# Kernel optimization log

Hardware: AMD Instinct MI355X
Metric: run time of the kernel (lower is better)

Reference implementation:

```python
import jax, jax.numpy as jnp
import numpy as np

N_NODES = 50000
N_EDGES = 500000
FEAT = 64
HEADS = 4


def setup_inputs() -> dict:
    key = jax.random.key(0)
    ks = jax.random.split(key, 8)
    x = jax.random.normal(ks[0], (N_NODES, FEAT), jnp.float32)
    edge_index = jax.random.randint(ks[1], (2, N_EDGES), 0, N_NODES)
    edge_vec = jax.random.normal(ks[2], (N_EDGES, 3), jnp.float32)
    edge_len = jax.random.uniform(ks[3], (N_EDGES,), jnp.float32)
    # learned parameters
    w_proj = jax.random.normal(ks[4], (HEADS, FEAT, FEAT), jnp.float32) / np.float32(np.sqrt(FEAT))
    xav = np.float32(np.sqrt(6.0 / (HEADS + FEAT)))
    radial_score = jax.random.uniform(ks[5], (HEADS, FEAT), jnp.float32, -xav, xav)
    tangential_score = jax.random.uniform(ks[6], (HEADS, FEAT), jnp.float32, -xav, xav)
    radial_distance_scale = jnp.array(1.0, jnp.float32)
    w_out = jax.random.normal(ks[7], (FEAT, FEAT), jnp.float32) / np.float32(np.sqrt(FEAT))
    return {
        "x": x,
        "edge_index": edge_index,
        "edge_vec": edge_vec,
        "edge_len": edge_len,
        "w_proj": w_proj,
        "radial_score": radial_score,
        "tangential_score": tangential_score,
        "radial_distance_scale": radial_distance_scale,
        "w_out": w_out,
    }


def reference(x, edge_index, edge_vec, edge_len, w_proj, radial_score,
              tangential_score, radial_distance_scale, w_out):
    # edge_vec is accepted by the original forward but never used.
    sender, receiver = edge_index[0], edge_index[1]
    num_nodes = x.shape[0]
    # per-head projection: [N,H,F]
    proj = jnp.einsum('nf,hfg->nhg', x, w_proj)
    # edge deltas: [E,H,F]
    delta = proj[sender] - proj[receiver]
    # logits: [E,H]
    radial_logits = jnp.einsum('ehf,hf->eh', delta, radial_score) \
        - radial_distance_scale * edge_len[:, None]
    tangential_logits = jnp.einsum('ehf,hf->eh', delta, tangential_score)

    def seg_softmax_msg(logits):
        # segment softmax over edges grouped by receiver (equivalent to the
        m = jax.ops.segment_max(logits, receiver, num_segments=num_nodes)  # [N,H]
        e = jnp.exp(logits - m[receiver])                                  # [E,H]
        s = jax.ops.segment_sum(e, receiver, num_segments=num_nodes)      # [N,H]
        alpha = e / s[receiver]                                            # [E,H]
        # weighted scatter-sum of deltas -> [N,H,F]
        return jax.ops.segment_sum(alpha[:, :, None] * delta, receiver,
                                   num_segments=num_nodes)

    out = (seg_softmax_msg(radial_logits) + seg_softmax_msg(tangential_logits))
    out = out.mean(axis=1)  # mean over heads -> [N,F]
    out = jnp.nan_to_num(out)
    return x + out @ w_out
```

## Files before the change

### kernel.cpp

```cpp
#include <hip/hip_runtime.h>

#define NN 50000
#define NE 500000
#define CAP 40

static __device__ __forceinline__ unsigned short f2b(float f) {
    union { float f; unsigned int u; } v; v.f = f;
    unsigned int u = v.u;
    unsigned int r = (u + 0x7FFFu + ((u >> 16) & 1u)) >> 16;
    return (unsigned short)r;
}
static __device__ __forceinline__ float b2f(unsigned short b) {
    union { unsigned int u; float f; } v; v.u = ((unsigned int)b) << 16;
    return v.f;
}
static __device__ __forceinline__ unsigned int pack2(float a, float b) {
    return (unsigned int)f2b(a) | ((unsigned int)f2b(b) << 16);
}

static __device__ __forceinline__ void finish_node(
    int n, float4 a, float4 r4, float4 t4, int lane, int h, int gq,
    float2* __restrict__ rst, unsigned short* __restrict__ projb)
{
    float pr = a.x * r4.x + a.y * r4.y + a.z * r4.z + a.w * r4.w;
    float pt = a.x * t4.x + a.y * t4.y + a.z * t4.z + a.w * t4.w;
    #pragma unroll
    for (int m = 1; m < 16; m <<= 1) {
        pr += __shfl_xor(pr, m);
        pt += __shfl_xor(pt, m);
    }
    if (gq == 0) rst[n * 4 + h] = make_float2(pr, pt);
    ushort4 pb;
    pb.x = f2b(a.x); pb.y = f2b(a.y); pb.z = f2b(a.z); pb.w = f2b(a.w);
    *((ushort4*)(projb + (size_t)n * 256 + lane * 4)) = pb;
}

__global__ __launch_bounds__(256) void k_proj(
    const float* __restrict__ x, const float* __restrict__ wp,
    const float* __restrict__ rsc, const float* __restrict__ tsc,
    unsigned short* __restrict__ projb, float2* __restrict__ rst,
    int* __restrict__ cnt)
{
    __shared__ float lw[4 * 64 * 64];
    int tid = threadIdx.x;
    int gtid = blockIdx.x * 256 + tid;
    if (gtid < NN) cnt[gtid] = 0;
    for (int i = tid; i < 4096; i += 256)
        ((float4*)lw)[i] = ((const float4*)wp)[i];
    __syncthreads();

    int lane = tid & 63, wid = tid >> 6;
    int h = lane >> 4, gq = lane & 15;
    const float4* wrow = (const float4*)(lw + h * 4096);
    float4 r4 = *(const float4*)(rsc + h * 64 + gq * 4);
    float4 t4 = *(const float4*)(tsc + h * 64 + gq * 4);

    int gw = blockIdx.x * 4 + wid;
    int n0 = gw * 4;
    if (n0 >= NN) return;
    float xv0 = x[(n0 + 0) * 64 + lane];
    float xv1 = x[(n0 + 1) * 64 + lane];
    float xv2 = x[(n0 + 2) * 64 + lane];
    float xv3 = x[(n0 + 3) * 64 + lane];
    float4 a0 = {0,0,0,0}, a1 = {0,0,0,0}, a2 = {0,0,0,0}, a3 = {0,0,0,0};
    #pragma unroll 4
    for (int k = 0; k < 64; ++k) {
        float4 w4 = wrow[k * 16 + gq];
        float k0 = __shfl(xv0, k), k1 = __shfl(xv1, k);
        float k2 = __shfl(xv2, k), k3 = __shfl(xv3, k);
        a0.x += k0 * w4.x; a0.y += k0 * w4.y; a0.z += k0 * w4.z; a0.w += k0 * w4.w;
        a1.x += k1 * w4.x; a1.y += k1 * w4.y; a1.z += k1 * w4.z; a1.w += k1 * w4.w;
        a2.x += k2 * w4.x; a2.y += k2 * w4.y; a2.z += k2 * w4.z; a2.w += k2 * w4.w;
        a3.x += k3 * w4.x; a3.y += k3 * w4.y; a3.z += k3 * w4.z; a3.w += k3 * w4.w;
    }
    finish_node(n0 + 0, a0, r4, t4, lane, h, gq, rst, projb);
    finish_node(n0 + 1, a1, r4, t4, lane, h, gq, rst, projb);
    finish_node(n0 + 2, a2, r4, t4, lane, h, gq, rst, projb);
    finish_node(n0 + 3, a3, r4, t4, lane, h, gq, rst, projb);
}

__global__ __launch_bounds__(256) void k_bucket(
    const int* __restrict__ ei, const float* __restrict__ elen,
    const float* __restrict__ rst_f,
    const float* __restrict__ scale_p,
    int* __restrict__ cnt, int* __restrict__ ssend, uint4* __restrict__ scrh)
{
    int e = blockIdx.x * 256 + threadIdx.x;
    if (e >= NE) return;
    int s = ei[e], r = ei[NE + e];
    float d = scale_p[0] * elen[e];
    float4 ss0 = *(const float4*)(rst_f + s * 8);
    float4 ss1 = *(const float4*)(rst_f + s * 8 + 4);
    float4 rr0 = *(const float4*)(rst_f + r * 8);
    float4 rr1 = *(const float4*)(rst_f + r * 8 + 4);
    int slot = atomicAdd(&cnt[r], 1);
    if (slot >= CAP) return;
    int idx = r * CAP + slot;
    ssend[idx] = s;
    uint4 rec;
    rec.x = pack2(__expf(ss0.x - rr0.x - d), __expf(ss0.y - rr0.y));
    rec.y = pack2(__expf(ss0.z - rr0.z - d), __expf(ss0.w - rr0.w));
    rec.z = pack2(__expf(ss1.x - rr1.x - d), __expf(ss1.y - rr1.y));
    rec.w = pack2(__expf(ss1.z - rr1.z - d), __expf(ss1.w - rr1.w));
    scrh[idx] = rec;
}

__global__ __launch_bounds__(256, 8) void k_msg(
    const float* __restrict__ x, const unsigned short* __restrict__ projb,
    const int* __restrict__ cnt, const int* __restrict__ ssend,
    const unsigned int* __restrict__ scrh_u,
    const float* __restrict__ wout, float* __restrict__ out)
{
    __shared__ float lwT[64 * 68];
    int tid = threadIdx.x;
    for (int i = tid; i < 4096; i += 256) {
        int f = i >> 6, g = i & 63;
        lwT[g * 68 + f] = wout[i];
    }

    int lane = tid & 63, wid = tid >> 6;
    int h = lane >> 4, q = lane & 15, grp = h << 4;
    int n = blockIdx.x * 4 + wid;

    float outv = x[n * 64 + lane];
    int cn = cnt[n]; if (cn > CAP) cn = CAP;

    float4 ar = {0.f,0.f,0.f,0.f}, at = {0.f,0.f,0.f,0.f};
    float srl = 0.f, stl = 0.f;

#define ROWLD(SJ) (*(const ushort4*)(projb + ((size_t)(SJ) << 8) + (lane << 2)))
#define CONS(P, IDX) { \
    float cr = __shfl(erq, grp + (IDX)); \
    float ct = __shfl(etq, grp + (IDX)); \
    float p0 = b2f((P).x), p1 = b2f((P).y), p2 = b2f((P).z), p3 = b2f((P).w); \
    ar.x += cr * p0; ar.y += cr * p1; ar.z += cr * p2; ar.w += cr * p3; \
    at.x += ct * p0; at.y += ct * p1; at.z += ct * p2; at.w += ct * p3; }

    if (cn > 0) {
        int rowb = n * CAP;
        for (int base = 0; base < cn; base += 12) {
            int bc = cn - base; if (bc > 12) bc = 12;
            int sv = ssend[rowb + base + q];
            unsigned cw = scrh_u[(size_t)(rowb + base + q) * 4 + h];
            int sq = (q < bc) ? sv : n;
            float erq = 0.f, etq = 0.f;
            if (q < bc) {
                erq = b2f((unsigned short)(cw & 0xffff));
                etq = b2f((unsigned short)(cw >> 16));
            }
            srl += erq; stl += etq;
            ushort4 pA = ROWLD(__shfl(sq, 0));
            ushort4 pB = ROWLD(__shfl(sq, 1));
            ushort4 pC = ROWLD(__shfl(sq, 2));
            ushort4 pD = ROWLD(__shfl(sq, 3));
            ushort4 pE = ROWLD(__shfl(sq, 4));
            ushort4 pF = ROWLD(__shfl(sq, 5));
            ushort4 pG = ROWLD(__shfl(sq, 6));
            ushort4 pH = ROWLD(__shfl(sq, 7));
            ushort4 pI = ROWLD(__shfl(sq, 8));
            ushort4 pJ = ROWLD(__shfl(sq, 9));
            ushort4 pK = ROWLD(__shfl(sq, 10));
            ushort4 pL = ROWLD(__shfl(sq, 11));
            CONS(pA, 0)  CONS(pB, 1)  CONS(pC, 2)  CONS(pD, 3)
            CONS(pE, 4)  CONS(pF, 5)  CONS(pG, 6)  CONS(pH, 7)
            CONS(pI, 8)  CONS(pJ, 9)  CONS(pK, 10) CONS(pL, 11)
        }
        #pragma unroll
        for (int m = 1; m < 16; m <<= 1) {
            srl += __shfl_xor(srl, m);
            stl += __shfl_xor(stl, m);
        }
        float isr = 1.0f / srl, ist = 1.0f / stl;
        ushort4 pr = ROWLD(n);
        ar.x = isr * ar.x + ist * at.x - 2.f * b2f(pr.x);
        ar.y = isr * ar.y + ist * at.y - 2.f * b2f(pr.y);
        ar.z = isr * ar.z + ist * at.z - 2.f * b2f(pr.z);
        ar.w = isr * ar.w + ist * at.w - 2.f * b2f(pr.w);
    }
    ar.x += __shfl_xor(ar.x, 16); ar.y += __shfl_xor(ar.y, 16);
    ar.z += __shfl_xor(ar.z, 16); ar.w += __shfl_xor(ar.w, 16);
    ar.x += __shfl_xor(ar.x, 32); ar.y += __shfl_xor(ar.y, 32);
    ar.z += __shfl_xor(ar.z, 32); ar.w += __shfl_xor(ar.w, 32);
    float4 m4 = make_float4(0.25f * ar.x, 0.25f * ar.y, 0.25f * ar.z, 0.25f * ar.w);

    __syncthreads();

    const float* wTg = lwT + lane * 68;
    #pragma unroll
    for (int j = 0; j < 16; ++j) {
        float4 wv = *(const float4*)(wTg + j * 4);
        outv += __shfl(m4.x, j) * wv.x + __shfl(m4.y, j) * wv.y
              + __shfl(m4.z, j) * wv.z + __shfl(m4.w, j) * wv.w;
    }
    out[n * 64 + lane] = outv;
#undef ROWLD
#undef CONS
}

extern "C" void kernel_launch(void* const* d_in, const int* in_sizes, int n_in,
                              void* d_out, int out_size, void* d_ws, size_t ws_size,
                              hipStream_t stream) {
    const float* x       = (const float*)d_in[0];
    const int*   ei      = (const int*)d_in[1];
    const float* elen    = (const float*)d_in[3];
    const float* wp      = (const float*)d_in[4];
    const float* rsc     = (const float*)d_in[5];
    const float* tsc     = (const float*)d_in[6];
    const float* scale_p = (const float*)d_in[7];
    const float* wout    = (const float*)d_in[8];
    float* out = (float*)d_out;

    char* ws = (char*)d_ws;
    size_t off = 0;
    auto alloc = [&](size_t bytes) {
        void* p = ws + off;
        off = (off + bytes + 255) & ~(size_t)255;
        return p;
    };
    unsigned short* projb = (unsigned short*)alloc((size_t)NN * 256 * 2);
    float2* rst   = (float2*)alloc((size_t)NN * 4 * 8);
    int*    cnt   = (int*)alloc((size_t)NN * 4);
    int*    ssend = (int*)alloc(((size_t)NN * CAP + 64) * 4);
    uint4*  scrh  = (uint4*)alloc(((size_t)NN * CAP + 64) * 16);

    k_proj<<<3125, 256, 0, stream>>>(x, wp, rsc, tsc, projb, rst, cnt);
    k_bucket<<<(NE + 255) / 256, 256, 0, stream>>>(ei, elen, (const float*)rst,
                                                   scale_p, cnt, ssend, scrh);
    k_msg<<<12500, 256, 0, stream>>>(x, projb, cnt, ssend,
                                     (const unsigned int*)scrh, wout, out);
}
```

Measured before the change: 271.7 us.

## Fuse projection, bucketing and message passing into one persistent grid-barrier kernel

```diff
diff --git a/kernel.cpp b/kernel.cpp
--- a/kernel.cpp
+++ b/kernel.cpp
@@ -3,12 +3,15 @@
 #define NN 50000
 #define NE 500000
 #define CAP 40
+#define NBLK 1024
+#define NTHR 256
+#define GSTRIDE (NBLK * NTHR)
+#define NWAVES (NBLK * 4)
 
 static __device__ __forceinline__ unsigned short f2b(float f) {
     union { float f; unsigned int u; } v; v.f = f;
     unsigned int u = v.u;
-    unsigned int r = (u + 0x7FFFu + ((u >> 16) & 1u)) >> 16;
-    return (unsigned short)r;
+    return (unsigned short)((u + 0x7FFFu + ((u >> 16) & 1u)) >> 16);
 }
 static __device__ __forceinline__ float b2f(unsigned short b) {
     union { unsigned int u; float f; } v; v.u = ((unsigned int)b) << 16;
@@ -18,115 +21,107 @@
     return (unsigned int)f2b(a) | ((unsigned int)f2b(b) << 16);
 }
 
-static __device__ __forceinline__ void finish_node(
-    int n, float4 a, float4 r4, float4 t4, int lane, int h, int gq,
-    float2* __restrict__ rst, unsigned short* __restrict__ projb)
-{
-    float pr = a.x * r4.x + a.y * r4.y + a.z * r4.z + a.w * r4.w;
-    float pt = a.x * t4.x + a.y * t4.y + a.z * t4.z + a.w * t4.w;
-    #pragma unroll
-    for (int m = 1; m < 16; m <<= 1) {
-        pr += __shfl_xor(pr, m);
-        pt += __shfl_xor(pt, m);
-    }
-    if (gq == 0) rst[n * 4 + h] = make_float2(pr, pt);
-    ushort4 pb;
-    pb.x = f2b(a.x); pb.y = f2b(a.y); pb.z = f2b(a.z); pb.w = f2b(a.w);
-    *((ushort4*)(projb + (size_t)n * 256 + lane * 4)) = pb;
-}
-
-__global__ __launch_bounds__(256) void k_proj(
-    const float* __restrict__ x, const float* __restrict__ wp,
+static __device__ __forceinline__ void grid_barrier(int* bar, int target) {
+    __syncthreads();
+    if (threadIdx.x == 0) {
+        __threadfence();
+        __hip_atomic_fetch_add(bar, 1, __ATOMIC_RELEASE, __HIP_MEMORY_SCOPE_AGENT);
+        while (__hip_atomic_load(bar, __ATOMIC_RELAXED, __HIP_MEMORY_SCOPE_AGENT) < target)
+            __builtin_amdgcn_s_sleep(8);
+        (void)__hip_atomic_load(bar, __ATOMIC_ACQUIRE, __HIP_MEMORY_SCOPE_AGENT);
+        __threadfence();
+    }
+    __syncthreads();
+}
+
+__global__ __launch_bounds__(NTHR, 4) void k_fused(
+    const float* __restrict__ x, const int* __restrict__ ei,
+    const float* __restrict__ elen, const float* __restrict__ wp,
     const float* __restrict__ rsc, const float* __restrict__ tsc,
+    const float* __restrict__ scale_p, const float* __restrict__ wout,
     unsigned short* __restrict__ projb, float2* __restrict__ rst,
-    int* __restrict__ cnt)
-{
-    __shared__ float lw[4 * 64 * 64];
-    int tid = threadIdx.x;
-    int gtid = blockIdx.x * 256 + tid;
-    if (gtid < NN) cnt[gtid] = 0;
-    for (int i = tid; i < 4096; i += 256)
-        ((float4*)lw)[i] = ((const float4*)wp)[i];
-    __syncthreads();
-
-    int lane = tid & 63, wid = tid >> 6;
-    int h = lane >> 4, gq = lane & 15;
-    const float4* wrow = (const float4*)(lw + h * 4096);
-    float4 r4 = *(const float4*)(rsc + h * 64 + gq * 4);
-    float4 t4 = *(const float4*)(tsc + h * 64 + gq * 4);
-
-    int gw = blockIdx.x * 4 + wid;
-    int n0 = gw * 4;
-    if (n0 >= NN) return;
-    float xv0 = x[(n0 + 0) * 64 + lane];
-    float xv1 = x[(n0 + 1) * 64 + lane];
-    float xv2 = x[(n0 + 2) * 64 + lane];
-    float xv3 = x[(n0 + 3) * 64 + lane];
-    float4 a0 = {0,0,0,0}, a1 = {0,0,0,0}, a2 = {0,0,0,0}, a3 = {0,0,0,0};
-    #pragma unroll 4
-    for (int k = 0; k < 64; ++k) {
-        float4 w4 = wrow[k * 16 + gq];
-        float k0 = __shfl(xv0, k), k1 = __shfl(xv1, k);
-        float k2 = __shfl(xv2, k), k3 = __shfl(xv3, k);
-        a0.x += k0 * w4.x; a0.y += k0 * w4.y; a0.z += k0 * w4.z; a0.w += k0 * w4.w;
-        a1.x += k1 * w4.x; a1.y += k1 * w4.y; a1.z += k1 * w4.z; a1.w += k1 * w4.w;
-        a2.x += k2 * w4.x; a2.y += k2 * w4.y; a2.z += k2 * w4.z; a2.w += k2 * w4.w;
-        a3.x += k3 * w4.x; a3.y += k3 * w4.y; a3.z += k3 * w4.z; a3.w += k3 * w4.w;
-    }
-    finish_node(n0 + 0, a0, r4, t4, lane, h, gq, rst, projb);
-    finish_node(n0 + 1, a1, r4, t4, lane, h, gq, rst, projb);
-    finish_node(n0 + 2, a2, r4, t4, lane, h, gq, rst, projb);
-    finish_node(n0 + 3, a3, r4, t4, lane, h, gq, rst, projb);
-}
-
-__global__ __launch_bounds__(256) void k_bucket(
-    const int* __restrict__ ei, const float* __restrict__ elen,
-    const float* __restrict__ rst_f,
-    const float* __restrict__ scale_p,
-    int* __restrict__ cnt, int* __restrict__ ssend, uint4* __restrict__ scrh)
-{
-    int e = blockIdx.x * 256 + threadIdx.x;
-    if (e >= NE) return;
-    int s = ei[e], r = ei[NE + e];
-    float d = scale_p[0] * elen[e];
-    float4 ss0 = *(const float4*)(rst_f + s * 8);
-    float4 ss1 = *(const float4*)(rst_f + s * 8 + 4);
-    float4 rr0 = *(const float4*)(rst_f + r * 8);
-    float4 rr1 = *(const float4*)(rst_f + r * 8 + 4);
-    int slot = atomicAdd(&cnt[r], 1);
-    if (slot >= CAP) return;
-    int idx = r * CAP + slot;
-    ssend[idx] = s;
-    uint4 rec;
-    rec.x = pack2(__expf(ss0.x - rr0.x - d), __expf(ss0.y - rr0.y));
-    rec.y = pack2(__expf(ss0.z - rr0.z - d), __expf(ss0.w - rr0.w));
-    rec.z = pack2(__expf(ss1.x - rr1.x - d), __expf(ss1.y - rr1.y));
-    rec.w = pack2(__expf(ss1.z - rr1.z - d), __expf(ss1.w - rr1.w));
-    scrh[idx] = rec;
-}
-
-__global__ __launch_bounds__(256, 8) void k_msg(
-    const float* __restrict__ x, const unsigned short* __restrict__ projb,
-    const int* __restrict__ cnt, const int* __restrict__ ssend,
-    const unsigned int* __restrict__ scrh_u,
-    const float* __restrict__ wout, float* __restrict__ out)
+    int* __restrict__ cnt, int* __restrict__ ssend,
+    unsigned int* __restrict__ scrh_u, int* __restrict__ bar,
+    float* __restrict__ out)
 {
     __shared__ float lwT[64 * 68];
-    int tid = threadIdx.x;
-    for (int i = tid; i < 4096; i += 256) {
+    const int tid = threadIdx.x, bid = blockIdx.x;
+    const int gtid = bid * NTHR + tid;
+    const int lane = tid & 63, wid = tid >> 6;
+    const int wgid = bid * 4 + wid;
+    const int h = lane >> 4, q = lane & 15, grp = h << 4;
+
+    for (int i = gtid; i < NN; i += GSTRIDE) cnt[i] = 0;
+    {
+        const float4* wrow = (const float4*)(wp + (size_t)h * 4096);
+        float4 r4 = *(const float4*)(rsc + h * 64 + q * 4);
+        float4 t4 = *(const float4*)(tsc + h * 64 + q * 4);
+        for (int g8 = wgid; g8 < NN / 8; g8 += NWAVES) {
+            int n0 = g8 * 8;
+            float xv[8]; float4 a[8];
+            #pragma unroll
+            for (int j = 0; j < 8; ++j) {
+                xv[j] = x[(n0 + j) * 64 + lane];
+                a[j] = make_float4(0.f, 0.f, 0.f, 0.f);
+            }
+            #pragma unroll 4
+            for (int k = 0; k < 64; ++k) {
+                float4 w4 = wrow[k * 16 + q];
+                #pragma unroll
+                for (int j = 0; j < 8; ++j) {
+                    float kx = __shfl(xv[j], k);
+                    a[j].x += kx * w4.x; a[j].y += kx * w4.y;
+                    a[j].z += kx * w4.z; a[j].w += kx * w4.w;
+                }
+            }
+            #pragma unroll
+            for (int j = 0; j < 8; ++j) {
+                int n = n0 + j;
+                float pr = a[j].x * r4.x + a[j].y * r4.y + a[j].z * r4.z + a[j].w * r4.w;
+                float pt = a[j].x * t4.x + a[j].y * t4.y + a[j].z * t4.z + a[j].w * t4.w;
+                #pragma unroll
+                for (int m = 1; m < 16; m <<= 1) {
+                    pr += __shfl_xor(pr, m);
+                    pt += __shfl_xor(pt, m);
+                }
+                if (q == 0) rst[n * 4 + h] = make_float2(pr, pt);
+                ushort4 pb;
+                pb.x = f2b(a[j].x); pb.y = f2b(a[j].y);
+                pb.z = f2b(a[j].z); pb.w = f2b(a[j].w);
+                *((ushort4*)(projb + (size_t)n * 256 + lane * 4)) = pb;
+            }
+        }
+    }
+    grid_barrier(bar, NBLK);
+
+    {
+        float sc = scale_p[0];
+        const float* sf = (const float*)rst;
+        for (int e = gtid; e < NE; e += GSTRIDE) {
+            int s = ei[e], r = ei[NE + e];
+            float d = sc * elen[e];
+            float4 ss0 = *(const float4*)(sf + s * 8);
+            float4 ss1 = *(const float4*)(sf + s * 8 + 4);
+            int slot = atomicAdd(&cnt[r], 1);
+            if (slot < CAP) {
+                int idx = r * CAP + slot;
+                ssend[idx] = s;
+                uint4 rec;
+                rec.x = pack2(__expf(ss0.x - d), __expf(ss0.y));
+                rec.y = pack2(__expf(ss0.z - d), __expf(ss0.w));
+                rec.z = pack2(__expf(ss1.x - d), __expf(ss1.y));
+                rec.w = pack2(__expf(ss1.z - d), __expf(ss1.w));
+                *((uint4*)(scrh_u + (size_t)idx * 4)) = rec;
+            }
+        }
+    }
+    grid_barrier(bar, 2 * NBLK);
+
+    for (int i = tid; i < 4096; i += NTHR) {
         int f = i >> 6, g = i & 63;
         lwT[g * 68 + f] = wout[i];
     }
-
-    int lane = tid & 63, wid = tid >> 6;
-    int h = lane >> 4, q = lane & 15, grp = h << 4;
-    int n = blockIdx.x * 4 + wid;
-
-    float outv = x[n * 64 + lane];
-    int cn = cnt[n]; if (cn > CAP) cn = CAP;
-
-    float4 ar = {0.f,0.f,0.f,0.f}, at = {0.f,0.f,0.f,0.f};
-    float srl = 0.f, stl = 0.f;
+    __syncthreads();
 
 #define ROWLD(SJ) (*(const ushort4*)(projb + ((size_t)(SJ) << 8) + (lane << 2)))
 #define CONS(P, IDX) { \
@@ -136,63 +131,70 @@
     ar.x += cr * p0; ar.y += cr * p1; ar.z += cr * p2; ar.w += cr * p3; \
     at.x += ct * p0; at.y += ct * p1; at.z += ct * p2; at.w += ct * p3; }
 
-    if (cn > 0) {
-        int rowb = n * CAP;
-        for (int base = 0; base < cn; base += 12) {
-            int bc = cn - base; if (bc > 12) bc = 12;
-            int sv = ssend[rowb + base + q];
-            unsigned cw = scrh_u[(size_t)(rowb + base + q) * 4 + h];
-            int sq = (q < bc) ? sv : n;
-            float erq = 0.f, etq = 0.f;
-            if (q < bc) {
-                erq = b2f((unsigned short)(cw & 0xffff));
-                etq = b2f((unsigned short)(cw >> 16));
-            }
-            srl += erq; stl += etq;
-            ushort4 pA = ROWLD(__shfl(sq, 0));
-            ushort4 pB = ROWLD(__shfl(sq, 1));
-            ushort4 pC = ROWLD(__shfl(sq, 2));
-            ushort4 pD = ROWLD(__shfl(sq, 3));
-            ushort4 pE = ROWLD(__shfl(sq, 4));
-            ushort4 pF = ROWLD(__shfl(sq, 5));
-            ushort4 pG = ROWLD(__shfl(sq, 6));
-            ushort4 pH = ROWLD(__shfl(sq, 7));
-            ushort4 pI = ROWLD(__shfl(sq, 8));
-            ushort4 pJ = ROWLD(__shfl(sq, 9));
-            ushort4 pK = ROWLD(__shfl(sq, 10));
-            ushort4 pL = ROWLD(__shfl(sq, 11));
-            CONS(pA, 0)  CONS(pB, 1)  CONS(pC, 2)  CONS(pD, 3)
-            CONS(pE, 4)  CONS(pF, 5)  CONS(pG, 6)  CONS(pH, 7)
-            CONS(pI, 8)  CONS(pJ, 9)  CONS(pK, 10) CONS(pL, 11)
-        }
+    for (int n = wgid; n < NN; n += NWAVES) {
+        float outv = x[n * 64 + lane];
+        int cn = __hip_atomic_load(&cnt[n], __ATOMIC_RELAXED, __HIP_MEMORY_SCOPE_AGENT);
+        if (cn > CAP) cn = CAP;
+        float4 ar = {0.f,0.f,0.f,0.f}, at = {0.f,0.f,0.f,0.f};
+        float srl = 0.f, stl = 0.f;
+        if (cn > 0) {
+            int rowb = n * CAP;
+            for (int base = 0; base < cn; base += 12) {
+                int bc = cn - base; if (bc > 12) bc = 12;
+                int idx = rowb + base + ((q < bc) ? q : (bc - 1));
+                int sq = __hip_atomic_load(&ssend[idx], __ATOMIC_RELAXED,
+                                           __HIP_MEMORY_SCOPE_AGENT);
+                unsigned cw = __hip_atomic_load(&scrh_u[(size_t)idx * 4 + h],
+                                                __ATOMIC_RELAXED, __HIP_MEMORY_SCOPE_AGENT);
+                float erq = 0.f, etq = 0.f;
+                if (q < bc) {
+                    erq = b2f((unsigned short)(cw & 0xffff));
+                    etq = b2f((unsigned short)(cw >> 16));
+                }
+                srl += erq; stl += etq;
+                ushort4 pA = ROWLD(__shfl(sq, 0));
+                ushort4 pB = ROWLD(__shfl(sq, 1));
+                ushort4 pC = ROWLD(__shfl(sq, 2));
+                ushort4 pD = ROWLD(__shfl(sq, 3));
+                ushort4 pE = ROWLD(__shfl(sq, 4));
+                ushort4 pF = ROWLD(__shfl(sq, 5));
+                ushort4 pG = ROWLD(__shfl(sq, 6));
+                ushort4 pH = ROWLD(__shfl(sq, 7));
+                ushort4 pI = ROWLD(__shfl(sq, 8));
+                ushort4 pJ = ROWLD(__shfl(sq, 9));
+                ushort4 pK = ROWLD(__shfl(sq, 10));
+                ushort4 pL = ROWLD(__shfl(sq, 11));
+                CONS(pA, 0)  CONS(pB, 1)  CONS(pC, 2)  CONS(pD, 3)
+                CONS(pE, 4)  CONS(pF, 5)  CONS(pG, 6)  CONS(pH, 7)
+                CONS(pI, 8)  CONS(pJ, 9)  CONS(pK, 10) CONS(pL, 11)
+            }
+            #pragma unroll
+            for (int m = 1; m < 16; m <<= 1) {
+                srl += __shfl_xor(srl, m);
+                stl += __shfl_xor(stl, m);
+            }
+            float isr = 1.0f / srl, ist = 1.0f / stl;
+            ushort4 pr = ROWLD(n);
+            ar.x = isr * ar.x + ist * at.x - 2.f * b2f(pr.x);
+            ar.y = isr * ar.y + ist * at.y - 2.f * b2f(pr.y);
+            ar.z = isr * ar.z + ist * at.z - 2.f * b2f(pr.z);
+            ar.w = isr * ar.w + ist * at.w - 2.f * b2f(pr.w);
+        }
+        ar.x += __shfl_xor(ar.x, 16); ar.y += __shfl_xor(ar.y, 16);
+        ar.z += __shfl_xor(ar.z, 16); ar.w += __shfl_xor(ar.w, 16);
+        ar.x += __shfl_xor(ar.x, 32); ar.y += __shfl_xor(ar.y, 32);
+        ar.z += __shfl_xor(ar.z, 32); ar.w += __shfl_xor(ar.w, 32);
+        float4 m4 = make_float4(0.25f * ar.x, 0.25f * ar.y, 0.25f * ar.z, 0.25f * ar.w);
+
+        const float* wTg = lwT + lane * 68;
         #pragma unroll
-        for (int m = 1; m < 16; m <<= 1) {
-            srl += __shfl_xor(srl, m);
-            stl += __shfl_xor(stl, m);
-        }
-        float isr = 1.0f / srl, ist = 1.0f / stl;
-        ushort4 pr = ROWLD(n);
-        ar.x = isr * ar.x + ist * at.x - 2.f * b2f(pr.x);
-        ar.y = isr * ar.y + ist * at.y - 2.f * b2f(pr.y);
-        ar.z = isr * ar.z + ist * at.z - 2.f * b2f(pr.z);
-        ar.w = isr * ar.w + ist * at.w - 2.f * b2f(pr.w);
-    }
-    ar.x += __shfl_xor(ar.x, 16); ar.y += __shfl_xor(ar.y, 16);
-    ar.z += __shfl_xor(ar.z, 16); ar.w += __shfl_xor(ar.w, 16);
-    ar.x += __shfl_xor(ar.x, 32); ar.y += __shfl_xor(ar.y, 32);
-    ar.z += __shfl_xor(ar.z, 32); ar.w += __shfl_xor(ar.w, 32);
-    float4 m4 = make_float4(0.25f * ar.x, 0.25f * ar.y, 0.25f * ar.z, 0.25f * ar.w);
-
-    __syncthreads();
-
-    const float* wTg = lwT + lane * 68;
-    #pragma unroll
-    for (int j = 0; j < 16; ++j) {
-        float4 wv = *(const float4*)(wTg + j * 4);
-        outv += __shfl(m4.x, j) * wv.x + __shfl(m4.y, j) * wv.y
-              + __shfl(m4.z, j) * wv.z + __shfl(m4.w, j) * wv.w;
-    }
-    out[n * 64 + lane] = outv;
+        for (int j = 0; j < 16; ++j) {
+            float4 wv = *(const float4*)(wTg + j * 4);
+            outv += __shfl(m4.x, j) * wv.x + __shfl(m4.y, j) * wv.y
+                  + __shfl(m4.z, j) * wv.z + __shfl(m4.w, j) * wv.w;
+        }
+        out[n * 64 + lane] = outv;
+    }
 #undef ROWLD
 #undef CONS
 }
@@ -218,14 +220,13 @@
         return p;
     };
     unsigned short* projb = (unsigned short*)alloc((size_t)NN * 256 * 2);
-    float2* rst   = (float2*)alloc((size_t)NN * 4 * 8);
-    int*    cnt   = (int*)alloc((size_t)NN * 4);
-    int*    ssend = (int*)alloc(((size_t)NN * CAP + 64) * 4);
-    uint4*  scrh  = (uint4*)alloc(((size_t)NN * CAP + 64) * 16);
-
-    k_proj<<<3125, 256, 0, stream>>>(x, wp, rsc, tsc, projb, rst, cnt);
-    k_bucket<<<(NE + 255) / 256, 256, 0, stream>>>(ei, elen, (const float*)rst,
-                                                   scale_p, cnt, ssend, scrh);
-    k_msg<<<12500, 256, 0, stream>>>(x, projb, cnt, ssend,
-                                     (const unsigned int*)scrh, wout, out);
-}
+    float2*       rst    = (float2*)alloc((size_t)NN * 4 * 8);
+    int*          cnt    = (int*)alloc((size_t)NN * 4);
+    int*          ssend  = (int*)alloc(((size_t)NN * CAP + 64) * 4);
+    unsigned int* scrh   = (unsigned int*)alloc(((size_t)NN * CAP + 64) * 16);
+    int*          bar    = (int*)alloc(256);
+
+    hipMemsetAsync(bar, 0, 16, stream);
+    k_fused<<<NBLK, NTHR, 0, stream>>>(x, ei, elen, wp, rsc, tsc, scale_p, wout,
+                                       projb, rst, cnt, ssend, scrh, bar, out);
+}
```

Result: slower. 610.7 us (+124.7%).

## Split output projection into separate kernel and drop receiver term from edge exponentials

Applied to the files above, without the earlier changes.

```diff
diff --git a/kernel.cpp b/kernel.cpp
--- a/kernel.cpp
+++ b/kernel.cpp
@@ -7,8 +7,7 @@
 static __device__ __forceinline__ unsigned short f2b(float f) {
     union { float f; unsigned int u; } v; v.f = f;
     unsigned int u = v.u;
-    unsigned int r = (u + 0x7FFFu + ((u >> 16) & 1u)) >> 16;
-    return (unsigned short)r;
+    return (unsigned short)((u + 0x7FFFu + ((u >> 16) & 1u)) >> 16);
 }
 static __device__ __forceinline__ float b2f(unsigned short b) {
     union { unsigned int u; float f; } v; v.u = ((unsigned int)b) << 16;
@@ -91,110 +90,115 @@
     float d = scale_p[0] * elen[e];
     float4 ss0 = *(const float4*)(rst_f + s * 8);
     float4 ss1 = *(const float4*)(rst_f + s * 8 + 4);
-    float4 rr0 = *(const float4*)(rst_f + r * 8);
-    float4 rr1 = *(const float4*)(rst_f + r * 8 + 4);
     int slot = atomicAdd(&cnt[r], 1);
     if (slot >= CAP) return;
     int idx = r * CAP + slot;
     ssend[idx] = s;
     uint4 rec;
-    rec.x = pack2(__expf(ss0.x - rr0.x - d), __expf(ss0.y - rr0.y));
-    rec.y = pack2(__expf(ss0.z - rr0.z - d), __expf(ss0.w - rr0.w));
-    rec.z = pack2(__expf(ss1.x - rr1.x - d), __expf(ss1.y - rr1.y));
-    rec.w = pack2(__expf(ss1.z - rr1.z - d), __expf(ss1.w - rr1.w));
+    rec.x = pack2(__expf(ss0.x - d), __expf(ss0.y));
+    rec.y = pack2(__expf(ss0.z - d), __expf(ss0.w));
+    rec.z = pack2(__expf(ss1.x - d), __expf(ss1.y));
+    rec.w = pack2(__expf(ss1.z - d), __expf(ss1.w));
     scrh[idx] = rec;
 }
 
-__global__ __launch_bounds__(256, 8) void k_msg(
-    const float* __restrict__ x, const unsigned short* __restrict__ projb,
+__global__ __launch_bounds__(256) void k_msg(
+    const unsigned short* __restrict__ projb,
     const int* __restrict__ cnt, const int* __restrict__ ssend,
     const unsigned int* __restrict__ scrh_u,
-    const float* __restrict__ wout, float* __restrict__ out)
-{
-    __shared__ float lwT[64 * 68];
+    unsigned short* __restrict__ msg)
+{
     int tid = threadIdx.x;
-    for (int i = tid; i < 4096; i += 256) {
-        int f = i >> 6, g = i & 63;
-        lwT[g * 68 + f] = wout[i];
-    }
-
     int lane = tid & 63, wid = tid >> 6;
-    int h = lane >> 4, q = lane & 15, grp = h << 4;
+    int h = lane >> 4, q = lane & 15;
     int n = blockIdx.x * 4 + wid;
 
-    float outv = x[n * 64 + lane];
     int cn = cnt[n]; if (cn > CAP) cn = CAP;
+    ushort4 own = *(const ushort4*)(projb + ((size_t)n << 8) + (lane << 2));
 
     float4 ar = {0.f,0.f,0.f,0.f}, at = {0.f,0.f,0.f,0.f};
     float srl = 0.f, stl = 0.f;
 
-#define ROWLD(SJ) (*(const ushort4*)(projb + ((size_t)(SJ) << 8) + (lane << 2)))
-#define CONS(P, IDX) { \
-    float cr = __shfl(erq, grp + (IDX)); \
-    float ct = __shfl(etq, grp + (IDX)); \
-    float p0 = b2f((P).x), p1 = b2f((P).y), p2 = b2f((P).z), p3 = b2f((P).w); \
-    ar.x += cr * p0; ar.y += cr * p1; ar.z += cr * p2; ar.w += cr * p3; \
-    at.x += ct * p0; at.y += ct * p1; at.z += ct * p2; at.w += ct * p3; }
-
     if (cn > 0) {
         int rowb = n * CAP;
-        for (int base = 0; base < cn; base += 12) {
-            int bc = cn - base; if (bc > 12) bc = 12;
-            int sv = ssend[rowb + base + q];
-            unsigned cw = scrh_u[(size_t)(rowb + base + q) * 4 + h];
-            int sq = (q < bc) ? sv : n;
-            float erq = 0.f, etq = 0.f;
-            if (q < bc) {
-                erq = b2f((unsigned short)(cw & 0xffff));
-                etq = b2f((unsigned short)(cw >> 16));
+        for (int base = 0; base < cn; base += 16) {
+            int bc = cn - base; if (bc > 16) bc = 16;
+            unsigned int cw[16]; int sq[16]; ushort4 pr[16];
+            #pragma unroll
+            for (int j = 0; j < 16; ++j) {
+                int jj = (j < bc) ? j : (bc - 1);
+                int idx = rowb + base + jj;
+                cw[j] = scrh_u[(size_t)idx * 4 + h];
+                sq[j] = ssend[idx];
             }
-            srl += erq; stl += etq;
-            ushort4 pA = ROWLD(__shfl(sq, 0));
-            ushort4 pB = ROWLD(__shfl(sq, 1));
-            ushort4 pC = ROWLD(__shfl(sq, 2));
-            ushort4 pD = ROWLD(__shfl(sq, 3));
-            ushort4 pE = ROWLD(__shfl(sq, 4));
-            ushort4 pF = ROWLD(__shfl(sq, 5));
-            ushort4 pG = ROWLD(__shfl(sq, 6));
-            ushort4 pH = ROWLD(__shfl(sq, 7));
-            ushort4 pI = ROWLD(__shfl(sq, 8));
-            ushort4 pJ = ROWLD(__shfl(sq, 9));
-            ushort4 pK = ROWLD(__shfl(sq, 10));
-            ushort4 pL = ROWLD(__shfl(sq, 11));
-            CONS(pA, 0)  CONS(pB, 1)  CONS(pC, 2)  CONS(pD, 3)
-            CONS(pE, 4)  CONS(pF, 5)  CONS(pG, 6)  CONS(pH, 7)
-            CONS(pI, 8)  CONS(pJ, 9)  CONS(pK, 10) CONS(pL, 11)
-        }
-        #pragma unroll
-        for (int m = 1; m < 16; m <<= 1) {
-            srl += __shfl_xor(srl, m);
-            stl += __shfl_xor(stl, m);
+            #pragma unroll
+            for (int j = 0; j < 16; ++j)
+                pr[j] = *(const ushort4*)(projb + ((size_t)sq[j] << 8) + (lane << 2));
+            #pragma unroll
+            for (int j = 0; j < 16; ++j) {
+                float er = 0.f, et = 0.f;
+                if (j < bc) {
+                    er = b2f((unsigned short)(cw[j] & 0xffffu));
+                    et = b2f((unsigned short)(cw[j] >> 16));
+                }
+                srl += er; stl += et;
+                float p0 = b2f(pr[j].x), p1 = b2f(pr[j].y);
+                float p2 = b2f(pr[j].z), p3 = b2f(pr[j].w);
+                ar.x += er * p0; ar.y += er * p1; ar.z += er * p2; ar.w += er * p3;
+                at.x += et * p0; at.y += et * p1; at.z += et * p2; at.w += et * p3;
+            }
         }
         float isr = 1.0f / srl, ist = 1.0f / stl;
-        ushort4 pr = ROWLD(n);
-        ar.x = isr * ar.x + ist * at.x - 2.f * b2f(pr.x);
-        ar.y = isr * ar.y + ist * at.y - 2.f * b2f(pr.y);
-        ar.z = isr * ar.z + ist * at.z - 2.f * b2f(pr.z);
-        ar.w = isr * ar.w + ist * at.w - 2.f * b2f(pr.w);
+        ar.x = isr * ar.x + ist * at.x - 2.f * b2f(own.x);
+        ar.y = isr * ar.y + ist * at.y - 2.f * b2f(own.y);
+        ar.z = isr * ar.z + ist * at.z - 2.f * b2f(own.z);
+        ar.w = isr * ar.w + ist * at.w - 2.f * b2f(own.w);
     }
     ar.x += __shfl_xor(ar.x, 16); ar.y += __shfl_xor(ar.y, 16);
     ar.z += __shfl_xor(ar.z, 16); ar.w += __shfl_xor(ar.w, 16);
     ar.x += __shfl_xor(ar.x, 32); ar.y += __shfl_xor(ar.y, 32);
     ar.z += __shfl_xor(ar.z, 32); ar.w += __shfl_xor(ar.w, 32);
-    float4 m4 = make_float4(0.25f * ar.x, 0.25f * ar.y, 0.25f * ar.z, 0.25f * ar.w);
-
-    __syncthreads();
-
-    const float* wTg = lwT + lane * 68;
+    if (h == 0) {
+        ushort4 mb;
+        mb.x = f2b(0.25f * ar.x); mb.y = f2b(0.25f * ar.y);
+        mb.z = f2b(0.25f * ar.z); mb.w = f2b(0.25f * ar.w);
+        *((ushort4*)(msg + (size_t)n * 64 + q * 4)) = mb;
+    }
+}
+
+__global__ __launch_bounds__(256) void k_out(
+    const float* __restrict__ x, const unsigned short* __restrict__ msg,
+    const float* __restrict__ wout, float* __restrict__ out)
+{
+    int lane = threadIdx.x & 63, wid = threadIdx.x >> 6;
+    float wreg[64];
     #pragma unroll
-    for (int j = 0; j < 16; ++j) {
-        float4 wv = *(const float4*)(wTg + j * 4);
-        outv += __shfl(m4.x, j) * wv.x + __shfl(m4.y, j) * wv.y
-              + __shfl(m4.z, j) * wv.z + __shfl(m4.w, j) * wv.w;
-    }
-    out[n * 64 + lane] = outv;
-#undef ROWLD
-#undef CONS
+    for (int f = 0; f < 64; ++f) wreg[f] = wout[f * 64 + lane];
+
+    int n0 = (blockIdx.x * 4 + wid) * 16;
+    for (int u = 0; u < 16; ++u) {
+        int n = n0 + u;
+        if (n >= NN) return;
+        float outv = x[(size_t)n * 64 + lane];
+        #pragma unroll
+        for (int j = 0; j < 8; ++j) {
+            uint2 mm = *(const uint2*)(msg + (size_t)n * 64 + j * 8);
+            float m0 = b2f((unsigned short)(mm.x & 0xffffu));
+            float m1 = b2f((unsigned short)(mm.x >> 16));
+            float m2 = b2f((unsigned short)(mm.y & 0xffffu));
+            float m3 = b2f((unsigned short)(mm.y >> 16));
+            outv += m0 * wreg[j * 8 + 0] + m1 * wreg[j * 8 + 1]
+                  + m2 * wreg[j * 8 + 2] + m3 * wreg[j * 8 + 3];
+            uint2 nn2 = *(const uint2*)(msg + (size_t)n * 64 + j * 8 + 4);
+            float m4 = b2f((unsigned short)(nn2.x & 0xffffu));
+            float m5 = b2f((unsigned short)(nn2.x >> 16));
+            float m6 = b2f((unsigned short)(nn2.y & 0xffffu));
+            float m7 = b2f((unsigned short)(nn2.y >> 16));
+            outv += m4 * wreg[j * 8 + 4] + m5 * wreg[j * 8 + 5]
+                  + m6 * wreg[j * 8 + 6] + m7 * wreg[j * 8 + 7];
+        }
+        out[(size_t)n * 64 + lane] = outv;
+    }
 }
 
 extern "C" void kernel_launch(void* const* d_in, const int* in_sizes, int n_in,
@@ -218,14 +222,16 @@
         return p;
     };
     unsigned short* projb = (unsigned short*)alloc((size_t)NN * 256 * 2);
-    float2* rst   = (float2*)alloc((size_t)NN * 4 * 8);
-    int*    cnt   = (int*)alloc((size_t)NN * 4);
-    int*    ssend = (int*)alloc(((size_t)NN * CAP + 64) * 4);
-    uint4*  scrh  = (uint4*)alloc(((size_t)NN * CAP + 64) * 16);
+    float2*         rst   = (float2*)alloc((size_t)NN * 4 * 8);
+    int*            cnt   = (int*)alloc((size_t)NN * 4);
+    int*            ssend = (int*)alloc(((size_t)NN * CAP + 64) * 4);
+    uint4*          scrh  = (uint4*)alloc(((size_t)NN * CAP + 64) * 16);
+    unsigned short* msg   = (unsigned short*)alloc((size_t)NN * 64 * 2);
 
     k_proj<<<3125, 256, 0, stream>>>(x, wp, rsc, tsc, projb, rst, cnt);
     k_bucket<<<(NE + 255) / 256, 256, 0, stream>>>(ei, elen, (const float*)rst,
                                                    scale_p, cnt, ssend, scrh);
-    k_msg<<<12500, 256, 0, stream>>>(x, projb, cnt, ssend,
-                                     (const unsigned int*)scrh, wout, out);
-}
+    k_msg<<<12500, 256, 0, stream>>>(projb, cnt, ssend,
+                                     (const unsigned int*)scrh, msg);
+    k_out<<<(NN + 63) / 64, 256, 0, stream>>>(x, msg, wout, out);
+}
```

Result: faster. 257.1 us (-5.4%).
